# Performance work log

Measured on AMD Instinct MI355X. Metric: run time of the kernel, lower is better.

Reference implementation:

```python
import jax, jax.numpy as jnp
import numpy as np


def setup_inputs() -> dict:
    key = jax.random.key(0)
    ks = jax.random.split(key, 8)
    B, N, C = 8, 4096, 128
    x = jax.random.normal(ks[0], (B, N, C), dtype=jnp.float32)
    spatial_pos = jax.random.randint(ks[1], (1, N, N), 0, 6, dtype=jnp.int32)
    sc = 1.0 / np.sqrt(C)
    W1 = jax.random.normal(ks[2], (C, C), dtype=jnp.float32) * sc
    b1 = jax.random.normal(ks[3], (C,), dtype=jnp.float32) * 0.01
    W2 = jax.random.normal(ks[4], (C, C // 8), dtype=jnp.float32) * sc
    b2 = jax.random.normal(ks[5], (C // 8,), dtype=jnp.float32) * 0.01
    Wb = jax.random.normal(ks[6], (C + C // 8, C), dtype=jnp.float32) * (1.0 / np.sqrt(C + C // 8))
    bb = jax.random.normal(ks[7], (C,), dtype=jnp.float32) * 0.01
    return {"x": x, "spatial_pos": spatial_pos, "W1": W1, "b1": b1,
            "W2": W2, "b2": b2, "Wb": Wb, "bb": bb}


def reference(x, spatial_pos, W1, b1, W2, b2, Wb, bb):
    # s=1, l=2: scale k=1 uses mask (spatial_pos <= 1), k=2 uses (spatial_pos == 2)
    sp = spatial_pos[0]                      # [N, N], batch-invariant
    m1 = (sp <= 1).astype(x.dtype)           # [N, N]
    m2 = (sp == 2).astype(x.dtype)           # [N, N]
    h1 = x @ W1 + b1                         # [B, N, C]
    h2 = x @ W2 + b2                         # [B, N, C//8]
    # torch.bmm(mask.expand(B,-1,-1), h) == einsum over shared mask
    f1 = jnp.einsum('ij,bjc->bic', m1, h1)   # [B, N, C]
    f2 = jnp.einsum('ij,bjc->bic', m2, h2)   # [B, N, C//8]
    feats = jnp.concatenate([f1, f2], axis=-1)  # [B, N, C + C//8]
    return feats @ Wb + bb                   # [B, N, output_dim]
```

## Files before the change

kernel.cpp:

```cpp
#include <hip/hip_runtime.h>
#include <stdint.h>

typedef unsigned short u16;
typedef __attribute__((ext_vector_type(8))) short short8;
typedef __attribute__((ext_vector_type(4))) float f32x4;
typedef __attribute__((ext_vector_type(16))) float f32x16;

#define MFMA __builtin_amdgcn_mfma_f32_16x16x32_bf16
#define MFMA32 __builtin_amdgcn_mfma_f32_32x32x16_bf16

__device__ __forceinline__ u16 f2bf(float f) {
  union { float f; uint32_t u; } v; v.f = f;
  return (u16)((v.u + 0x7FFFu + ((v.u >> 16) & 1u)) >> 16);
}

#define GLOAD16(gp, lp) \
  __builtin_amdgcn_global_load_lds((const __attribute__((address_space(1))) uint32_t*)(gp), \
                                   (__attribute__((address_space(3))) uint32_t*)(lp), 16, 0, 0)

#define WS_H    0
#define WS_Q1   9502720
#define WS_Q2   9503232
#define WS_M1P  9503744
#define WS_M2P  11600896
#define WS_RS1  13698048
#define WS_RS2  13714432
#define WS_WSB  13730816

__global__ __launch_bounds__(256) void k0(const int* __restrict__ sp,
                                          unsigned long long* __restrict__ m1p,
                                          unsigned long long* __restrict__ m2p,
                                          float* __restrict__ rs1, float* __restrict__ rs2,
                                          const float* __restrict__ W1, const float* __restrict__ Wb,
                                          const float* __restrict__ b1, const float* __restrict__ b2,
                                          const float* __restrict__ W2,
                                          float* __restrict__ q1, float* __restrict__ q2,
                                          u16* __restrict__ wsbg) {
  const int tid = threadIdx.x;
  if (blockIdx.x < 1024) {
    int wave = tid >> 6, lane = tid & 63;
    int i = blockIdx.x * 4 + wave;
    const int* rowp = sp + (size_t)i * 4096;
    int c1 = 0, c2 = 0;
    for (int w = 0; w < 64; ++w) {
      int v = rowp[w * 64 + lane];
      unsigned long long bb1 = __ballot(v <= 1);
      unsigned long long bb2 = __ballot(v == 2);
      if (lane == 0) {
        m1p[(size_t)w * 4096 + i] = bb1;
        m2p[(size_t)w * 4096 + i] = bb2;
        c1 += __popcll(bb1);
        c2 += __popcll(bb2);
      }
    }
    if (lane == 0) { rs1[i] = (float)c1; rs2[i] = (float)c2; }
    return;
  }
  int idx = (int)(blockIdx.x - 1024) * 256 + tid;
  int a = idx >> 7, c = idx & 127;
  float acc = 0.f;
  for (int k = 0; k < 128; ++k) acc += W1[a * 128 + k] * Wb[k * 128 + c];
  wsbg[(((a >> 3) * 144) + c) * 8 + (a & 7)] = f2bf(acc);
  if (idx < 2048) {
    int k = idx >> 4, nn2 = idx & 15;
    wsbg[(((k >> 3) * 144) + 128 + nn2) * 8 + (k & 7)] = f2bf(W2[k * 16 + nn2]);
  }
  if (idx < 128) {
    float s1 = 0.f, s2 = 0.f;
    for (int k = 0; k < 128; ++k) s1 += b1[k] * Wb[k * 128 + idx];
    for (int k = 0; k < 16; ++k)  s2 += b2[k] * Wb[(128 + k) * 128 + idx];
    q1[idx] = s1; q2[idx] = s2;
  }
}

__global__ __launch_bounds__(256, 2) void kproj(const float* __restrict__ x,
                                                const u16* __restrict__ wsbg,
                                                u16* __restrict__ H) {
  __shared__ u16 wsb[18432];
  __shared__ u16 xs[64 * 136];
  __shared__ u16 hs[64 * 146];
  const int tid = threadIdx.x;
  const int bid = blockIdx.x;
  const int b = bid >> 6;
  const int kt = bid & 63;
  const size_t r0 = (size_t)b * 4096 + (size_t)kt * 64;

#pragma unroll
  for (int i = 0; i < 9; ++i)
    GLOAD16(wsbg + (i * 256 + tid) * 8, (char*)&wsb[0] + (i * 256 + tid) * 16);
  {
    const float* xp = x + (r0 + (tid >> 2)) * 128 + (tid & 3) * 32;
    u16* xd = xs + (tid >> 2) * 136 + (tid & 3) * 32;
#pragma unroll
    for (int i = 0; i < 4; ++i) {
      f32x4 a = ((const f32x4*)xp)[i * 2];
      f32x4 bq = ((const f32x4*)xp)[i * 2 + 1];
      short8 pk;
      pk[0] = (short)f2bf(a[0]); pk[1] = (short)f2bf(a[1]);
      pk[2] = (short)f2bf(a[2]); pk[3] = (short)f2bf(a[3]);
      pk[4] = (short)f2bf(bq[0]); pk[5] = (short)f2bf(bq[1]);
      pk[6] = (short)f2bf(bq[2]); pk[7] = (short)f2bf(bq[3]);
      *(short8*)(xd + i * 8) = pk;
    }
  }
  __syncthreads();

  const int w = tid >> 6, l = tid & 63, lr = l & 15, lg = l >> 4;
  f32x4 acc[9];
  f32x4 zz = {0.f, 0.f, 0.f, 0.f};
#pragma unroll
  for (int fn = 0; fn < 9; ++fn) acc[fn] = zz;
#pragma unroll
  for (int kf = 0; kf < 4; ++kf) {
    short8 af = *(const short8*)(xs + (w * 16 + lr) * 136 + kf * 32 + lg * 8);
#pragma unroll
    for (int fn = 0; fn < 9; ++fn) {
      short8 bf = *(const short8*)(wsb + (((kf * 4 + lg) * 144) + fn * 16 + lr) * 8);
      acc[fn] = MFMA(af, bf, acc[fn], 0, 0, 0);
    }
  }
  __syncthreads();
#pragma unroll
  for (int fn = 0; fn < 9; ++fn)
#pragma unroll
    for (int g = 0; g < 4; ++g)
      hs[(w * 16 + lg * 4 + g) * 146 + fn * 16 + lr] = f2bf(acc[fn][g]);
  __syncthreads();
  const size_t base = (size_t)kt * 73728 + (size_t)b * 9216;
  for (int i = 0; i < 5; ++i) {
    int ch = i * 256 + tid;
    if (ch < 1152) {
      union { u16 s[8]; uint4 v; } pk;
      size_t di;
      if (ch < 1024) {
        int cb = ch >> 8, ks = (ch >> 6) & 3, ll = ch & 63;
        int row = ks * 16 + (ll >> 5) * 8;
        int col = cb * 32 + (ll & 31);
#pragma unroll
        for (int e = 0; e < 8; ++e) pk.s[e] = hs[(row + e) * 146 + col];
        di = base + (size_t)((cb * 4 + ks) * 512 + ll * 8);
      } else {
        int c2 = ch - 1024;
        int kf = c2 >> 6, ll = c2 & 63;
        int row = kf * 32 + (ll >> 4) * 8;
        int col = 128 + (ll & 15);
#pragma unroll
        for (int e = 0; e < 8; ++e) pk.s[e] = hs[(row + e) * 146 + col];
        di = base + (size_t)(8192 + kf * 512 + ll * 8);
      }
      *(uint4*)(H + di) = pk.v;
    }
  }
}

__device__ __forceinline__ short8 expand_byte(uint32_t wd, int sh) {
  uint32_t b = (wd >> sh) & 0xFFu;
  uint32_t t = b * 0x8001u;
  union { uint32_t u[4]; short8 s; } r;
  r.u[0] = (t & 0x00010001u) * 0x3F80u;
  r.u[1] = (t & 0x00040004u) * 0x0FE0u;
  r.u[2] = (t & 0x00100010u) * 0x03F8u;
  r.u[3] = (t & 0x00400040u) * 0x00FEu;
  return r.s;
}

__global__ __launch_bounds__(512, 2) void kb1(const u16* __restrict__ H,
                                              const char* __restrict__ M1b,
                                              const char* __restrict__ M2b,
                                              const float* __restrict__ rs1, const float* __restrict__ rs2,
                                              const float* __restrict__ q1, const float* __restrict__ q2,
                                              const float* __restrict__ Wb, const float* __restrict__ bb,
                                              float* __restrict__ out) {
  __shared__ u16 bt[3][9216];
  __shared__ u16 mkb[3][1024];
  __shared__ u16 f2s[128 * 40];
  __shared__ u16 wb2s[2048];

  const int tid = threadIdx.x;
  const int bid = blockIdx.x;
  const int b = bid & 7;
  const int i0 = (bid >> 3) * 128;

  const int w = tid >> 6, l = tid & 63, lr = l & 15, lg = l >> 4;
  const int h = w >> 1, c2 = w & 1;
  const int cb0 = c2 * 2, cb1 = c2 * 2 + 1;
  const int sh32 = (l >> 5) * 8;
  const int lgsh = lg * 8;

  const u16* pB0 = H + (size_t)b * 9216 + (size_t)tid * 8;
  const u16* pB1 = H + (size_t)b * 9216 + (size_t)(512 + tid) * 8;
  const u16* pB2 = H + (size_t)b * 9216 + (size_t)(1024 + tid) * 8;
  const int mc = tid - 128;
  const char* pM = ((mc & 64) ? M2b : M1b) + (size_t)i0 * 8 + (size_t)(mc & 63) * 16;
  const int dB0 = tid * 16, dB1 = (512 + tid) * 16, dB2 = (1024 + tid) * 16;
  const int dM = ((mc >> 6) & 1) * 1024 + (mc & 63) * 16;

#define STAGE(BUF) { \
    GLOAD16(pB0, (char*)&bt[BUF][0] + dB0); \
    GLOAD16(pB1, (char*)&bt[BUF][0] + dB1); \
    if (tid < 128) GLOAD16(pB2, (char*)&bt[BUF][0] + dB2); \
    else if (tid < 256) GLOAD16(pM, (char*)&mkb[BUF][0] + dM); \
    pB0 += 73728; pB1 += 73728; pB2 += 73728; pM += 32768; }

  const int fb0 = (cb0 * 4) * 512 + l * 8;
  const int fb1 = (cb1 * 4) * 512 + l * 8;
  const int fm0 = 8192 + l * 8;
  const int fm1 = 8192 + 512 + l * 8;

  f32x16 am0, am1;
  f32x4 acc2;
#pragma unroll
  for (int i = 0; i < 16; ++i) { am0[i] = 0.f; am1[i] = 0.f; }
  acc2[0] = acc2[1] = acc2[2] = acc2[3] = 0.f;

#define WAITV { if (w < 4) asm volatile("s_waitcnt vmcnt(3)" ::: "memory"); \
                else asm volatile("s_waitcnt vmcnt(2)" ::: "memory"); }

#define COMPUTE(BUF) { \
    const u16* src_ = &bt[BUF][0]; \
    const char* mk_ = (const char*)&mkb[BUF][0]; \
    uint2 c1_ = *(const uint2*)(mk_ + (h * 32 + (l & 31)) * 8); \
    uint2 cm_ = *(const uint2*)(mk_ + 1024 + (w * 16 + lr) * 8); \
    short8 bA0_ = *(const short8*)(src_ + fb0); \
    short8 bA1_ = *(const short8*)(src_ + fb0 + 512); \
    short8 bA2_ = *(const short8*)(src_ + fb0 + 1024); \
    short8 bA3_ = *(const short8*)(src_ + fb0 + 1536); \
    short8 bB0_ = *(const short8*)(src_ + fb1); \
    short8 bB1_ = *(const short8*)(src_ + fb1 + 512); \
    short8 bB2_ = *(const short8*)(src_ + fb1 + 1024); \
    short8 bB3_ = *(const short8*)(src_ + fb1 + 1536); \
    short8 bm0_ = *(const short8*)(src_ + fm0); \
    short8 bm1_ = *(const short8*)(src_ + fm1); \
    short8 e0_ = expand_byte(c1_.x, sh32); \
    short8 e1_ = expand_byte(c1_.x, sh32 + 16); \
    short8 e2_ = expand_byte(c1_.y, sh32); \
    short8 e3_ = expand_byte(c1_.y, sh32 + 16); \
    short8 em0_ = expand_byte(cm_.x, lgsh); \
    short8 em1_ = expand_byte(cm_.y, lgsh); \
    __builtin_amdgcn_s_setprio(1); \
    am0 = MFMA32(e0_, bA0_, am0, 0, 0, 0); \
    am1 = MFMA32(e0_, bB0_, am1, 0, 0, 0); \
    am0 = MFMA32(e1_, bA1_, am0, 0, 0, 0); \
    am1 = MFMA32(e1_, bB1_, am1, 0, 0, 0); \
    am0 = MFMA32(e2_, bA2_, am0, 0, 0, 0); \
    am1 = MFMA32(e2_, bB2_, am1, 0, 0, 0); \
    am0 = MFMA32(e3_, bA3_, am0, 0, 0, 0); \
    am1 = MFMA32(e3_, bB3_, am1, 0, 0, 0); \
    acc2 = MFMA(em0_, bm0_, acc2, 0, 0, 0); \
    acc2 = MFMA(em1_, bm1_, acc2, 0, 0, 0); \
    __builtin_amdgcn_s_setprio(0); }

#define PHASE(BUF, BUF2) { WAITV; __builtin_amdgcn_s_barrier(); STAGE(BUF2); COMPUTE(BUF) }

  STAGE(0);
  STAGE(1);

#pragma unroll
  for (int i = 0; i < 4; ++i) {
    int e = i * 512 + tid;
    int cb = e >> 9, rem = e & 511, ll = rem >> 3, ee = rem & 7;
    wb2s[e] = f2bf(Wb[(128 + (ll >> 5) * 8 + ee) * 128 + cb * 32 + (ll & 31)]);
  }

  for (int it = 0; it < 20; ++it) {
    PHASE(0, 2);
    PHASE(1, 0);
    PHASE(2, 1);
  }
  PHASE(0, 2);
  PHASE(1, 0);
  { WAITV; __builtin_amdgcn_s_barrier(); COMPUTE(2) }
  { asm volatile("s_waitcnt vmcnt(0)" ::: "memory");
    __builtin_amdgcn_s_barrier(); COMPUTE(0) }

#pragma unroll
  for (int gg = 0; gg < 4; ++gg)
    f2s[(w * 16 + lg * 4 + gg) * 40 + lr] = f2bf(acc2[gg]);
  __syncthreads();

  {
    short8 af = *(const short8*)(f2s + (h * 32 + (l & 31)) * 40 + (l >> 5) * 8);
    short8 bw0 = *(const short8*)(wb2s + cb0 * 512 + l * 8);
    short8 bw1 = *(const short8*)(wb2s + cb1 * 512 + l * 8);
    am0 = MFMA32(af, bw0, am0, 0, 0, 0);
    am1 = MFMA32(af, bw1, am1, 0, 0, 0);
  }

  const int col0 = cb0 * 32 + (l & 31), col1 = cb1 * 32 + (l & 31);
  const float q10 = q1[col0], q20 = q2[col0], bb0 = bb[col0];
  const float q11 = q1[col1], q21 = q2[col1], bb1 = bb[col1];
#pragma unroll
  for (int r = 0; r < 16; ++r) {
    int row = h * 32 + (r & 3) + 8 * (r >> 2) + 4 * (l >> 5);
    float r1 = rs1[i0 + row], r2 = rs2[i0 + row];
    size_t obase = ((size_t)b * 4096 + i0 + row) * 128;
    out[obase + col0] = am0[r] + r1 * q10 + r2 * q20 + bb0;
    out[obase + col1] = am1[r] + r1 * q11 + r2 * q21 + bb1;
  }
}

extern "C" void kernel_launch(void* const* d_in, const int* in_sizes, int n_in,
                              void* d_out, int out_size, void* d_ws, size_t ws_size,
                              hipStream_t stream) {
  const float* x  = (const float*)d_in[0];
  const int*   sp = (const int*)d_in[1];
  const float* W1 = (const float*)d_in[2];
  const float* b1 = (const float*)d_in[3];
  const float* W2 = (const float*)d_in[4];
  const float* b2 = (const float*)d_in[5];
  const float* Wb = (const float*)d_in[6];
  const float* bb = (const float*)d_in[7];
  float* out = (float*)d_out;
  char* ws = (char*)d_ws;

  u16* H = (u16*)(ws + WS_H);
  float* q1 = (float*)(ws + WS_Q1);
  float* q2 = (float*)(ws + WS_Q2);
  unsigned long long* m1p = (unsigned long long*)(ws + WS_M1P);
  unsigned long long* m2p = (unsigned long long*)(ws + WS_M2P);
  float* rs1 = (float*)(ws + WS_RS1);
  float* rs2 = (float*)(ws + WS_RS2);
  u16* wsbg = (u16*)(ws + WS_WSB);

  k0<<<1088, 256, 0, stream>>>(sp, m1p, m2p, rs1, rs2, W1, Wb, b1, b2, W2, q1, q2, wsbg);
  kproj<<<512, 256, 0, stream>>>(x, wsbg, H);
  kb1<<<256, 512, 0, stream>>>(H, (const char*)m1p, (const char*)m2p,
                               rs1, rs2, q1, q2, Wb, bb, out);
}
```

Measured before the change: 89.24 us.

## Remap warp tiling so each warp shares B fragments across two row groups

```diff
diff --git a/kernel.cpp b/kernel.cpp
--- a/kernel.cpp
+++ b/kernel.cpp
@@ -173,6 +173,7 @@
                                               float* __restrict__ out) {
   __shared__ u16 bt[3][9216];
   __shared__ u16 mkb[3][1024];
+  __shared__ float f2pf[2][128][16];
   __shared__ u16 f2s[128 * 40];
   __shared__ u16 wb2s[2048];
 
@@ -182,8 +183,10 @@
   const int i0 = (bid >> 3) * 128;
 
   const int w = tid >> 6, l = tid & 63, lr = l & 15, lg = l >> 4;
-  const int h = w >> 1, c2 = w & 1;
-  const int cb0 = c2 * 2, cb1 = c2 * 2 + 1;
+  const int h2 = w >> 2, cb = w & 3;
+  const int rg0 = h2 * 2, rg1 = h2 * 2 + 1;
+  const int kfm = h2;
+  const int rt0 = cb * 2, rt1 = cb * 2 + 1;
   const int sh32 = (l >> 5) * 8;
   const int lgsh = lg * 8;
 
@@ -202,16 +205,15 @@
     else if (tid < 256) GLOAD16(pM, (char*)&mkb[BUF][0] + dM); \
     pB0 += 73728; pB1 += 73728; pB2 += 73728; pM += 32768; }
 
-  const int fb0 = (cb0 * 4) * 512 + l * 8;
-  const int fb1 = (cb1 * 4) * 512 + l * 8;
-  const int fm0 = 8192 + l * 8;
-  const int fm1 = 8192 + 512 + l * 8;
+  const int fb0 = (cb * 4) * 512 + l * 8;
+  const int fm0 = 8192 + kfm * 512 + l * 8;
 
   f32x16 am0, am1;
-  f32x4 acc2;
+  f32x4 acc2a, acc2b;
 #pragma unroll
   for (int i = 0; i < 16; ++i) { am0[i] = 0.f; am1[i] = 0.f; }
-  acc2[0] = acc2[1] = acc2[2] = acc2[3] = 0.f;
+  acc2a[0] = acc2a[1] = acc2a[2] = acc2a[3] = 0.f;
+  acc2b[0] = acc2b[1] = acc2b[2] = acc2b[3] = 0.f;
 
 #define WAITV { if (w < 4) asm volatile("s_waitcnt vmcnt(3)" ::: "memory"); \
                 else asm volatile("s_waitcnt vmcnt(2)" ::: "memory"); }
@@ -219,35 +221,36 @@
 #define COMPUTE(BUF) { \
     const u16* src_ = &bt[BUF][0]; \
     const char* mk_ = (const char*)&mkb[BUF][0]; \
-    uint2 c1_ = *(const uint2*)(mk_ + (h * 32 + (l & 31)) * 8); \
-    uint2 cm_ = *(const uint2*)(mk_ + 1024 + (w * 16 + lr) * 8); \
-    short8 bA0_ = *(const short8*)(src_ + fb0); \
-    short8 bA1_ = *(const short8*)(src_ + fb0 + 512); \
-    short8 bA2_ = *(const short8*)(src_ + fb0 + 1024); \
-    short8 bA3_ = *(const short8*)(src_ + fb0 + 1536); \
-    short8 bB0_ = *(const short8*)(src_ + fb1); \
-    short8 bB1_ = *(const short8*)(src_ + fb1 + 512); \
-    short8 bB2_ = *(const short8*)(src_ + fb1 + 1024); \
-    short8 bB3_ = *(const short8*)(src_ + fb1 + 1536); \
-    short8 bm0_ = *(const short8*)(src_ + fm0); \
-    short8 bm1_ = *(const short8*)(src_ + fm1); \
-    short8 e0_ = expand_byte(c1_.x, sh32); \
-    short8 e1_ = expand_byte(c1_.x, sh32 + 16); \
-    short8 e2_ = expand_byte(c1_.y, sh32); \
-    short8 e3_ = expand_byte(c1_.y, sh32 + 16); \
-    short8 em0_ = expand_byte(cm_.x, lgsh); \
-    short8 em1_ = expand_byte(cm_.y, lgsh); \
+    uint2 cA_ = *(const uint2*)(mk_ + (rg0 * 32 + (l & 31)) * 8); \
+    uint2 cB_ = *(const uint2*)(mk_ + (rg1 * 32 + (l & 31)) * 8); \
+    uint32_t cm0_ = *(const uint32_t*)(mk_ + 1024 + (rt0 * 16 + lr) * 8 + kfm * 4); \
+    uint32_t cm1_ = *(const uint32_t*)(mk_ + 1024 + (rt1 * 16 + lr) * 8 + kfm * 4); \
+    short8 bf0_ = *(const short8*)(src_ + fb0); \
+    short8 bf1_ = *(const short8*)(src_ + fb0 + 512); \
+    short8 bf2_ = *(const short8*)(src_ + fb0 + 1024); \
+    short8 bf3_ = *(const short8*)(src_ + fb0 + 1536); \
+    short8 bm_  = *(const short8*)(src_ + fm0); \
+    short8 eA0_ = expand_byte(cA_.x, sh32); \
+    short8 eA1_ = expand_byte(cA_.x, sh32 + 16); \
+    short8 eA2_ = expand_byte(cA_.y, sh32); \
+    short8 eA3_ = expand_byte(cA_.y, sh32 + 16); \
+    short8 eB0_ = expand_byte(cB_.x, sh32); \
+    short8 eB1_ = expand_byte(cB_.x, sh32 + 16); \
+    short8 eB2_ = expand_byte(cB_.y, sh32); \
+    short8 eB3_ = expand_byte(cB_.y, sh32 + 16); \
+    short8 em0_ = expand_byte(cm0_, lgsh); \
+    short8 em1_ = expand_byte(cm1_, lgsh); \
     __builtin_amdgcn_s_setprio(1); \
-    am0 = MFMA32(e0_, bA0_, am0, 0, 0, 0); \
-    am1 = MFMA32(e0_, bB0_, am1, 0, 0, 0); \
-    am0 = MFMA32(e1_, bA1_, am0, 0, 0, 0); \
-    am1 = MFMA32(e1_, bB1_, am1, 0, 0, 0); \
-    am0 = MFMA32(e2_, bA2_, am0, 0, 0, 0); \
-    am1 = MFMA32(e2_, bB2_, am1, 0, 0, 0); \
-    am0 = MFMA32(e3_, bA3_, am0, 0, 0, 0); \
-    am1 = MFMA32(e3_, bB3_, am1, 0, 0, 0); \
-    acc2 = MFMA(em0_, bm0_, acc2, 0, 0, 0); \
-    acc2 = MFMA(em1_, bm1_, acc2, 0, 0, 0); \
+    am0 = MFMA32(eA0_, bf0_, am0, 0, 0, 0); \
+    am1 = MFMA32(eB0_, bf0_, am1, 0, 0, 0); \
+    am0 = MFMA32(eA1_, bf1_, am0, 0, 0, 0); \
+    am1 = MFMA32(eB1_, bf1_, am1, 0, 0, 0); \
+    am0 = MFMA32(eA2_, bf2_, am0, 0, 0, 0); \
+    am1 = MFMA32(eB2_, bf2_, am1, 0, 0, 0); \
+    am0 = MFMA32(eA3_, bf3_, am0, 0, 0, 0); \
+    am1 = MFMA32(eB3_, bf3_, am1, 0, 0, 0); \
+    acc2a = MFMA(em0_, bm_, acc2a, 0, 0, 0); \
+    acc2b = MFMA(em1_, bm_, acc2b, 0, 0, 0); \
     __builtin_amdgcn_s_setprio(0); }
 
 #define PHASE(BUF, BUF2) { WAITV; __builtin_amdgcn_s_barrier(); STAGE(BUF2); COMPUTE(BUF) }
@@ -258,8 +261,8 @@
 #pragma unroll
   for (int i = 0; i < 4; ++i) {
     int e = i * 512 + tid;
-    int cb = e >> 9, rem = e & 511, ll = rem >> 3, ee = rem & 7;
-    wb2s[e] = f2bf(Wb[(128 + (ll >> 5) * 8 + ee) * 128 + cb * 32 + (ll & 31)]);
+    int cbw = e >> 9, rem = e & 511, ll = rem >> 3, ee = rem & 7;
+    wb2s[e] = f2bf(Wb[(128 + (ll >> 5) * 8 + ee) * 128 + cbw * 32 + (ll & 31)]);
   }
 
   for (int it = 0; it < 20; ++it) {
@@ -274,28 +277,42 @@
     __builtin_amdgcn_s_barrier(); COMPUTE(0) }
 
 #pragma unroll
-  for (int gg = 0; gg < 4; ++gg)
-    f2s[(w * 16 + lg * 4 + gg) * 40 + lr] = f2bf(acc2[gg]);
+  for (int gg = 0; gg < 4; ++gg) {
+    f2pf[kfm][rt0 * 16 + lg * 4 + gg][lr] = acc2a[gg];
+    f2pf[kfm][rt1 * 16 + lg * 4 + gg][lr] = acc2b[gg];
+  }
+  __syncthreads();
+#pragma unroll
+  for (int j = 0; j < 4; ++j) {
+    int e = j * 512 + tid;
+    int row = e >> 4, col = e & 15;
+    f2s[row * 40 + col] = f2bf(f2pf[0][row][col] + f2pf[1][row][col]);
+  }
   __syncthreads();
 
   {
-    short8 af = *(const short8*)(f2s + (h * 32 + (l & 31)) * 40 + (l >> 5) * 8);
-    short8 bw0 = *(const short8*)(wb2s + cb0 * 512 + l * 8);
-    short8 bw1 = *(const short8*)(wb2s + cb1 * 512 + l * 8);
-    am0 = MFMA32(af, bw0, am0, 0, 0, 0);
-    am1 = MFMA32(af, bw1, am1, 0, 0, 0);
-  }
-
-  const int col0 = cb0 * 32 + (l & 31), col1 = cb1 * 32 + (l & 31);
-  const float q10 = q1[col0], q20 = q2[col0], bb0 = bb[col0];
-  const float q11 = q1[col1], q21 = q2[col1], bb1 = bb[col1];
+    short8 bw_ = *(const short8*)(wb2s + cb * 512 + l * 8);
+    short8 afA = *(const short8*)(f2s + (rg0 * 32 + (l & 31)) * 40 + sh32);
+    short8 afB = *(const short8*)(f2s + (rg1 * 32 + (l & 31)) * 40 + sh32);
+    am0 = MFMA32(afA, bw_, am0, 0, 0, 0);
+    am1 = MFMA32(afB, bw_, am1, 0, 0, 0);
+  }
+
+  const int colA = cb * 32 + (l & 31);
+  const float q1v = q1[colA], q2v = q2[colA], bbv = bb[colA];
 #pragma unroll
   for (int r = 0; r < 16; ++r) {
-    int row = h * 32 + (r & 3) + 8 * (r >> 2) + 4 * (l >> 5);
-    float r1 = rs1[i0 + row], r2 = rs2[i0 + row];
-    size_t obase = ((size_t)b * 4096 + i0 + row) * 128;
-    out[obase + col0] = am0[r] + r1 * q10 + r2 * q20 + bb0;
-    out[obase + col1] = am1[r] + r1 * q11 + r2 * q21 + bb1;
+    int rr = (r & 3) + 8 * (r >> 2) + 4 * (l >> 5);
+    {
+      int row = rg0 * 32 + rr;
+      float r1 = rs1[i0 + row], r2 = rs2[i0 + row];
+      out[((size_t)b * 4096 + i0 + row) * 128 + colA] = am0[r] + r1 * q1v + r2 * q2v + bbv;
+    }
+    {
+      int row = rg1 * 32 + rr;
+      float r1 = rs1[i0 + row], r2 = rs2[i0 + row];
+      out[((size_t)b * 4096 + i0 + row) * 128 + colA] = am1[r] + r1 * q1v + r2 * q2v + bbv;
+    }
   }
 }
 
```

New measurement: 97.00 us. 1.09x slower.
